# Kernel tuning notes

Hardware: AMD Instinct MI355X
Metric: run time of the kernel (lower is better)

Reference implementation:

```python
import jax, jax.numpy as jnp
import numpy as np

A = 8      # action_channels
K = 3      # receptive_field
PAD = K // 2
PAD_VALUE = 0.0
B, H, W = 32, 160, 160


def setup_inputs() -> dict:
    key = jax.random.key(0)
    k1, k2, k3 = jax.random.split(key, 3)
    values = jax.random.normal(k1, (B, 1, H, W), dtype=jnp.float32)
    rewards = jax.random.normal(k2, (B, 1, H, W), dtype=jnp.float32)
    # Conv2d(1, A*K*K, K, bias=False) weight, PyTorch-style kaiming-ish scale
    weight = jax.random.normal(k3, (A * K * K, 1, K, K), dtype=jnp.float32) * (1.0 / K)
    return {"values": values, "rewards": rewards, "weight": weight}


def reference(values, rewards, weight):
    rv = values + rewards                                   # [B,1,H,W]
    rv_p = jnp.pad(rv, ((0, 0), (0, 0), (PAD, PAD), (PAD, PAD)),
                   constant_values=PAD_VALUE)               # [B,1,H+2p,W+2p]

    # dynamic per-pixel transition logits: conv2d -> [B, A*K*K, H, W]
    dyn = jax.lax.conv_general_dilated(
        rv_p, weight, window_strides=(1, 1), padding='VALID',
        dimension_numbers=('NCHW', 'OIHW', 'NCHW'))
    # rearrange 'b (o i k1 k2) h w -> b o h w (i k1 k2)' with i=1
    dyn = dyn.reshape(B, A, K * K, H, W).transpose(0, 1, 3, 4, 2)  # [B,A,H,W,KK]
    dyn = jax.nn.softmax(dyn, axis=-1)

    # F.unfold(pad(rv), K): 9 shifted views, row-major (k1, k2) order -> [B,KK,H,W]
    x = rv_p[:, 0]                                           # [B,H+2p,W+2p]
    patches = jnp.stack([x[:, di:di + H, dj:dj + W]
                         for di in range(K) for dj in range(K)], axis=1)

    # einsum 'b i h w, b o h w i -> b o h w'
    q_values = jnp.einsum('bihw,bohwi->bohw', patches, dyn)  # [B,A,H,W]

    # hard maxpool over action dim
    return q_values.max(axis=1, keepdims=True)               # [B,1,H,W]
```

## Files before the change

### kernel.cpp

```cpp
#include <hip/hip_runtime.h>
#include <math.h>

typedef float f32x2 __attribute__((ext_vector_type(2)));

#define A_HEADS 8
#define BB 32
#define HH 160
#define WW 160
#define LOG2E 1.44269504088896340736f

#if __has_builtin(__builtin_amdgcn_exp2f)
#define EXP2RAW(x) __builtin_amdgcn_exp2f(x)
#else
static __device__ __forceinline__ float EXP2RAW(float x) {
    float r;
    asm("v_exp_f32 %0, %1" : "=v"(r) : "v"(x));
    return r;
}
#endif

__global__ __launch_bounds__(256) void vi_kernel(
    const float* __restrict__ values,
    const float* __restrict__ rewards,
    const float* __restrict__ weight,
    float* __restrict__ out)
{
    int w  = blockIdx.x * 32 + threadIdx.x;
    int hb = blockIdx.y * 8 + threadIdx.y;
    int h  = hb % HH;
    int b  = hb / HH;

    const float* vbase = values  + b * (HH * WW);
    const float* rbase = rewards + b * (HH * WW);

    float patch[9];
    #pragma unroll
    for (int di = 0; di < 3; ++di) {
        int hh = h + di - 1;
        bool hok = (hh >= 0) && (hh < HH);
        #pragma unroll
        for (int dj = 0; dj < 3; ++dj) {
            int ww = w + dj - 1;
            bool ok = hok && (ww >= 0) && (ww < WW);
            float val = 0.0f;
            if (ok) {
                int off = hh * WW + ww;
                val = vbase[off] + rbase[off];
            }
            patch[di * 3 + dj] = val;
        }
    }

    float pls[9];
    #pragma unroll
    for (int j = 0; j < 9; ++j) pls[j] = patch[j] * LOG2E;
    f32x2 pp2[4];
    #pragma unroll
    for (int j2 = 0; j2 < 4; ++j2)
        pp2[j2] = (f32x2){patch[2 * j2], patch[2 * j2 + 1]};

    float best = -INFINITY;
    #pragma unroll
    for (int a = 0; a < A_HEADS; ++a) {
        f32x2 den2 = (f32x2){0.0f, 0.0f};
        f32x2 num2 = (f32x2){0.0f, 0.0f};
        #pragma unroll
        for (int i2 = 0; i2 < 4; ++i2) {
            const float* w0 = weight + (a * 9 + 2 * i2) * 9;
            f32x2 acc2 = (f32x2){0.0f, 0.0f};
            #pragma unroll
            for (int j = 0; j < 9; ++j) {
                f32x2 wp = (f32x2){w0[j], w0[j + 9]};
                acc2 = __builtin_elementwise_fma((f32x2){pls[j], pls[j]}, wp, acc2);
            }
            f32x2 e2;
            e2.x = EXP2RAW(acc2.x);
            e2.y = EXP2RAW(acc2.y);
            den2 += e2;
            num2 = __builtin_elementwise_fma(pp2[i2], e2, num2);
        }
        {
            const float* w8 = weight + (a * 9 + 8) * 9;
            float acc8 = 0.0f;
            #pragma unroll
            for (int j = 0; j < 9; ++j) acc8 = fmaf(pls[j], w8[j], acc8);
            float e8 = EXP2RAW(acc8);
            float den = den2.x + den2.y + e8;
            float num = num2.x + num2.y;
            num = fmaf(patch[8], e8, num);
            best = fmaxf(best, num * __builtin_amdgcn_rcpf(den));
        }
    }

    out[hb * WW + w] = best;
}

extern "C" void kernel_launch(void* const* d_in, const int* in_sizes, int n_in,
                              void* d_out, int out_size, void* d_ws, size_t ws_size,
                              hipStream_t stream)
{
    const float* values  = (const float*)d_in[0];
    const float* rewards = (const float*)d_in[1];
    const float* weight  = (const float*)d_in[2];
    float* out = (float*)d_out;

    dim3 block(32, 8);
    dim3 grid(WW / 32, (BB * HH) / 8);
    vi_kernel<<<grid, block, 0, stream>>>(values, rewards, weight, out);
}
```

Before: 24.17 us.

## Split action heads across thread pairs and pack two heads per f32x2

Each pixel is now handled by two threads, each computing four of the eight action heads, with a cross-lane shuffle combining their maxima before one thread writes. Inside a thread, two heads are processed in lockstep using packed f32x2 FMAs over all nine taps, replacing the earlier packing of tap pairs with a scalar leftover tap. This doubles the thread count to expose more parallelism and removes the odd-tap scalar path, at the cost of loading and adding the input patch twice and running an extra shuffle.

Result: slower. 67.55 us (+179.5%).

```diff
diff --git a/kernel.cpp b/kernel.cpp
--- a/kernel.cpp
+++ b/kernel.cpp
@@ -26,7 +26,9 @@
     float* __restrict__ out)
 {
     int w  = blockIdx.x * 32 + threadIdx.x;
-    int hb = blockIdx.y * 8 + threadIdx.y;
+    int u  = blockIdx.y * 8 + threadIdx.y;
+    int hb = u >> 1;
+    int hs = u & 1;
     int h  = hb % HH;
     int b  = hb / HH;
 
@@ -54,45 +56,38 @@
     float pls[9];
     #pragma unroll
     for (int j = 0; j < 9; ++j) pls[j] = patch[j] * LOG2E;
-    f32x2 pp2[4];
-    #pragma unroll
-    for (int j2 = 0; j2 < 4; ++j2)
-        pp2[j2] = (f32x2){patch[2 * j2], patch[2 * j2 + 1]};
 
     float best = -INFINITY;
     #pragma unroll
-    for (int a = 0; a < A_HEADS; ++a) {
+    for (int ap = 0; ap < 2; ++ap) {
+        const float* wbase0 = weight + ((hs * 4 + 2 * ap) * 9) * 9;
         f32x2 den2 = (f32x2){0.0f, 0.0f};
         f32x2 num2 = (f32x2){0.0f, 0.0f};
         #pragma unroll
-        for (int i2 = 0; i2 < 4; ++i2) {
-            const float* w0 = weight + (a * 9 + 2 * i2) * 9;
+        for (int i = 0; i < 9; ++i) {
+            const float* wr = wbase0 + i * 9;
             f32x2 acc2 = (f32x2){0.0f, 0.0f};
             #pragma unroll
             for (int j = 0; j < 9; ++j) {
-                f32x2 wp = (f32x2){w0[j], w0[j + 9]};
+                f32x2 wp = (f32x2){wr[j], wr[j + 81]};
                 acc2 = __builtin_elementwise_fma((f32x2){pls[j], pls[j]}, wp, acc2);
             }
             f32x2 e2;
             e2.x = EXP2RAW(acc2.x);
             e2.y = EXP2RAW(acc2.y);
             den2 += e2;
-            num2 = __builtin_elementwise_fma(pp2[i2], e2, num2);
+            num2 = __builtin_elementwise_fma((f32x2){patch[i], patch[i]}, e2, num2);
         }
-        {
-            const float* w8 = weight + (a * 9 + 8) * 9;
-            float acc8 = 0.0f;
-            #pragma unroll
-            for (int j = 0; j < 9; ++j) acc8 = fmaf(pls[j], w8[j], acc8);
-            float e8 = EXP2RAW(acc8);
-            float den = den2.x + den2.y + e8;
-            float num = num2.x + num2.y;
-            num = fmaf(patch[8], e8, num);
-            best = fmaxf(best, num * __builtin_amdgcn_rcpf(den));
-        }
+        float q0 = num2.x * __builtin_amdgcn_rcpf(den2.x);
+        float q1 = num2.y * __builtin_amdgcn_rcpf(den2.y);
+        best = fmaxf(best, fmaxf(q0, q1));
     }
 
-    out[hb * WW + w] = best;
+    float other = __shfl_xor(best, 32);
+    best = fmaxf(best, other);
+    if (hs == 0) {
+        out[hb * WW + w] = best;
+    }
 }
 
 extern "C" void kernel_launch(void* const* d_in, const int* in_sizes, int n_in,
@@ -105,6 +100,6 @@
     float* out = (float*)d_out;
 
     dim3 block(32, 8);
-    dim3 grid(WW / 32, (BB * HH) / 8);
+    dim3 grid(WW / 32, 2 * (BB * HH) / 8);
     vi_kernel<<<grid, block, 0, stream>>>(values, rewards, weight, out);
 }
```
